# Kernel tuning notes

Hardware: AMD Instinct MI355X
Metric: run time of the kernel (lower is better)

## Reference

```python
import jax, jax.numpy as jnp
import numpy as np

N = 50000
NEG_SLOPE = 0.2  # PyG GATConv default negative_slope


def _gat_layer(x, src, dst, edge_attr, W, We, a_src, a_dst, a_edge, bias):
    """Single-head PyG GATConv (heads=1, concat=True, add_self_loops=True,
    fill_value='mean' for self-loop edge_attr, dropout inactive / eval mode)."""
    n = x.shape[0]
    # add self loops; self-loop edge_attr = per-feature mean of edge_attr
    loop = jnp.arange(n)
    src2 = jnp.concatenate([src, loop])
    dst2 = jnp.concatenate([dst, loop])
    ea_loop = jnp.broadcast_to(edge_attr.mean(axis=0, keepdims=True), (n, edge_attr.shape[1]))
    ea = jnp.concatenate([edge_attr, ea_loop], axis=0)          # [E', edge_dim]

    h = x @ W                                                    # [N, C_out]
    a_s = h @ a_src                                              # [N]
    a_d = h @ a_dst                                              # [N]
    a_e = (ea @ We) @ a_edge                                     # [E']

    alpha = jax.nn.leaky_relu(a_s[src2] + a_d[dst2] + a_e, NEG_SLOPE)  # [E']
    # segment softmax over incoming edges of each dst node
    amax = jax.ops.segment_max(alpha, dst2, num_segments=n)     # [N]
    ex = jnp.exp(alpha - amax[dst2])                             # [E']
    denom = jax.ops.segment_sum(ex, dst2, num_segments=n)       # [N]
    w = ex / denom[dst2]                                         # [E']

    msg = h[src2] * w[:, None]                                   # [E', C_out]
    out = jax.ops.segment_sum(msg, dst2, num_segments=n) + bias  # [N, C_out]
    return out


def setup_inputs() -> dict:
    key = jax.random.key(0)
    ks = jax.random.split(key, 16)
    E, C_in, C_h, C_out, Ed = 800000, 128, 256, 128, 8
    s = 0.05
    inp = {
        "x": jax.random.normal(ks[0], (N, C_in), dtype=jnp.float32),
        "edge_index": jax.random.randint(ks[1], (2, E), 0, N, dtype=jnp.int32),
        "edge_attr": jax.random.normal(ks[2], (E, Ed), dtype=jnp.float32),
        # layer 1 params
        "W1": jax.random.normal(ks[3], (C_in, C_h), dtype=jnp.float32) * s,
        "We1": jax.random.normal(ks[4], (Ed, C_h), dtype=jnp.float32) * s,
        "as1": jax.random.normal(ks[5], (C_h,), dtype=jnp.float32) * s,
        "ad1": jax.random.normal(ks[6], (C_h,), dtype=jnp.float32) * s,
        "ae1": jax.random.normal(ks[7], (C_h,), dtype=jnp.float32) * s,
        "b1": jnp.zeros((C_h,), dtype=jnp.float32),
        # layer 2 params
        "W2": jax.random.normal(ks[8], (C_h, C_out), dtype=jnp.float32) * s,
        "We2": jax.random.normal(ks[9], (Ed, C_out), dtype=jnp.float32) * s,
        "as2": jax.random.normal(ks[10], (C_out,), dtype=jnp.float32) * s,
        "ad2": jax.random.normal(ks[11], (C_out,), dtype=jnp.float32) * s,
        "ae2": jax.random.normal(ks[12], (C_out,), dtype=jnp.float32) * s,
        "b2": jnp.zeros((C_out,), dtype=jnp.float32),
    }
    return inp


def reference(x, edge_index, edge_attr, W1, We1, as1, ad1, ae1, b1,
              W2, We2, as2, ad2, ae2, b2):
    src, dst = edge_index[0], edge_index[1]
    h = _gat_layer(x, src, dst, edge_attr, W1, We1, as1, ad1, ae1, b1)
    h = jax.nn.relu(h)  # relu between layers, not after last
    out = _gat_layer(h, src, dst, edge_attr, W2, We2, as2, ad2, ae2, b2)
    return out
```

## Files before the change

### kernel.cpp

```cpp
#include <hip/hip_runtime.h>
#include <hip/hip_bf16.h>


#define NEG_SLOPE 0.2f
#define EHB 2048

typedef unsigned short u16;
typedef short short8 __attribute__((ext_vector_type(8)));
typedef float v4f __attribute__((ext_vector_type(4)));
typedef u16 u16x4 __attribute__((ext_vector_type(4)));
typedef u16 u16x8 __attribute__((ext_vector_type(8)));

__device__ __forceinline__ u16 f2bf(float f) {
    unsigned u = __float_as_uint(f);
    return (u16)((u + 0x7fffu + ((u >> 16) & 1u)) >> 16);
}
__device__ __forceinline__ float bf2f(u16 h) {
    return __uint_as_float(((unsigned)h) << 16);
}
__device__ __forceinline__ float bf_lo(int v) { return __uint_as_float(((unsigned)v) << 16); }
__device__ __forceinline__ float bf_hi(int v) { return __uint_as_float(((unsigned)v) & 0xffff0000u); }
__device__ __forceinline__ float lrelu(float x) {
    return x >= 0.f ? x : NEG_SLOPE * x;
}
__device__ __forceinline__ int ld_acq(int* p) {
    return __hip_atomic_load(p, __ATOMIC_ACQUIRE, __HIP_MEMORY_SCOPE_AGENT);
}
__device__ __forceinline__ void st_rel(int* p, int v) {
    __hip_atomic_store(p, v, __ATOMIC_RELEASE, __HIP_MEMORY_SCOPE_AGENT);
}

__global__ __launch_bounds__(256) void pre_fat_kernel(
        const float* __restrict__ ea, const int* __restrict__ dst,
        const float* __restrict__ We1, const float* __restrict__ ae1v,
        const float* __restrict__ We2, const float* __restrict__ ae2v,
        float* __restrict__ mean_acc, int* __restrict__ deg,
        int* __restrict__ rank,
        float2* __restrict__ aEe, int E,
        const float* __restrict__ W1, u16* __restrict__ w1thi, u16* __restrict__ w1tlo,
        const float* __restrict__ W2, u16* __restrict__ w2thi, u16* __restrict__ w2tlo,
        float* __restrict__ we_vec1g, float* __restrict__ we_vec2g) {
    int tid = threadIdx.x;
    if (blockIdx.x >= EHB) {
        int t = (blockIdx.x - EHB) * 256 + tid;
        if (t < 128 * 256) {
            int k = t >> 8, m = t & 255;
            float v = W1[t];
            u16 h = f2bf(v);
            w1thi[(size_t)m * 128 + k] = h;
            w1tlo[(size_t)m * 128 + k] = f2bf(v - bf2f(h));
        } else {
            t -= 128 * 256;
            int k = t >> 7, m = t & 127;
            float v = W2[t];
            u16 h = f2bf(v);
            w2thi[(size_t)m * 256 + k] = h;
            w2tlo[(size_t)m * 256 + k] = f2bf(v - bf2f(h));
        }
        return;
    }
    __shared__ float red[8];
    __shared__ float wv[16];
    if (tid < 16) { wv[tid] = 0.f; if (tid < 8) red[tid] = 0.f; }
    __syncthreads();
    {
        float a1 = ae1v[tid];
        int lane = tid & 63;
#pragma unroll
        for (int j = 0; j < 8; ++j) {
            float v = We1[j * 256 + tid] * a1;
#pragma unroll
            for (int o = 32; o; o >>= 1) v += __shfl_down(v, o);
            if (lane == 0) atomicAdd(&wv[j], v);
        }
        if (tid < 128) {
            float a2 = ae2v[tid];
#pragma unroll
            for (int j = 0; j < 8; ++j) {
                float v = We2[j * 128 + tid] * a2;
#pragma unroll
                for (int o = 32; o; o >>= 1) v += __shfl_down(v, o);
                if (lane == 0) atomicAdd(&wv[8 + j], v);
            }
        }
    }
    __syncthreads();
    if (blockIdx.x == 0 && tid < 16) {
        if (tid < 8) we_vec1g[tid] = wv[tid];
        else         we_vec2g[tid - 8] = wv[tid];
    }
    float s[8] = {0.f};
    int stride = EHB * 256;
    for (int e = blockIdx.x * 256 + tid; e < E; e += stride) {
        int d = dst[e];
        rank[e] = atomicAdd(&deg[d], 1);
        const float4 v0 = *(const float4*)&ea[(size_t)e * 8];
        const float4 v1 = *(const float4*)&ea[(size_t)e * 8 + 4];
        s[0] += v0.x; s[1] += v0.y; s[2] += v0.z; s[3] += v0.w;
        s[4] += v1.x; s[5] += v1.y; s[6] += v1.z; s[7] += v1.w;
        float s1 = v0.x * wv[0] + v0.y * wv[1] + v0.z * wv[2] + v0.w * wv[3]
                 + v1.x * wv[4] + v1.y * wv[5] + v1.z * wv[6] + v1.w * wv[7];
        float s2 = v0.x * wv[8] + v0.y * wv[9] + v0.z * wv[10] + v0.w * wv[11]
                 + v1.x * wv[12] + v1.y * wv[13] + v1.z * wv[14] + v1.w * wv[15];
        aEe[e] = make_float2(s1, s2);
    }
#pragma unroll
    for (int j = 0; j < 8; ++j) atomicAdd(&red[j], s[j]);
    __syncthreads();
    if (tid < 8) atomicAdd(&mean_acc[tid], red[tid]);
}

__global__ __launch_bounds__(256) void scan_fused_kernel(
        const int* __restrict__ deg, int* __restrict__ row_start,
        int* __restrict__ partials, int* __restrict__ pprefix,
        int* __restrict__ gcount, int* __restrict__ gflag, int N, int n,
        const float* __restrict__ mean_acc, float Einv,
        const float* __restrict__ we_vec1, const float* __restrict__ we_vec2,
        float* __restrict__ ae_loop) {
    __shared__ int s[256];
    __shared__ int amLast, bprefix;
    int t = threadIdx.x, bid = blockIdx.x;
    int i = bid * 256 + t;
    int v = (i < N) ? deg[i] : 0;
    s[t] = v; __syncthreads();
    for (int off = 1; off < 256; off <<= 1) {
        int u = (t >= off) ? s[t - off] : 0;
        __syncthreads();
        s[t] += u;
        __syncthreads();
    }
    int incl = s[t];
    int total = s[255];
    if (t == 0) {
        partials[bid] = total;
        __threadfence();
        int c = __hip_atomic_fetch_add(gcount, 1, __ATOMIC_ACQ_REL, __HIP_MEMORY_SCOPE_AGENT);
        amLast = (c == (int)gridDim.x - 1);
    }
    __syncthreads();
    if (amLast) {
        int G = gridDim.x;
        int pv = (t < G) ? ld_acq(&partials[t]) : 0;
        __syncthreads();
        s[t] = pv; __syncthreads();
        for (int off = 1; off < 256; off <<= 1) {
            int u = (t >= off) ? s[t - off] : 0;
            __syncthreads();
            s[t] += u;
            __syncthreads();
        }
        if (t < G) pprefix[t] = s[t] - pv;
        if (t == 0) {
            float s1 = 0.f, s2 = 0.f;
#pragma unroll
            for (int j = 0; j < 8; ++j) {
                float m = mean_acc[j] * Einv;
                s1 += m * we_vec1[j];
                s2 += m * we_vec2[j];
            }
            ae_loop[0] = s1; ae_loop[1] = s2;
        }
        __threadfence();
        __syncthreads();
        if (t == 0) st_rel(gflag, 1);
    }
    if (t == 0) {
        while (ld_acq(gflag) == 0) __builtin_amdgcn_s_sleep(2);
        bprefix = ld_acq(&pprefix[bid]);
    }
    __syncthreads();
    int ex = bprefix + incl - v;
    if (i < n) row_start[i] = ex;
}

#define BK 32
#define LDA 40
__global__ __launch_bounds__(256) void gemm1_fill_fat_kernel(
        const float* __restrict__ A32,
        const u16* __restrict__ Bh_g, const u16* __restrict__ Bl_g,
        u16* __restrict__ Cb, int Nrows, int K, int M,
        const float* __restrict__ av, const float* __restrict__ bv,
        float* __restrict__ as_out, float* __restrict__ ad_out, int Gg, int gx,
        const int* __restrict__ src, const int* __restrict__ dst,
        const float2* __restrict__ aEe, const int* __restrict__ row_start,
        const int* __restrict__ rank,
        float4* __restrict__ epack, int E) {
    __shared__ u16 Ah[128 * LDA], Bh[128 * LDA], Bl[128 * LDA];
    int tid = threadIdx.x;
    if ((int)blockIdx.x >= Gg) {
        int e = ((int)blockIdx.x - Gg) * 256 + tid;
        if (e < E) {
            int d = dst[e];
            int idx = row_start[d] + rank[e];
            float2 a = aEe[e];
            epack[idx] = make_float4(__int_as_float(src[e]), a.x, a.y, 0.f);
        }
        return;
    }
    int lane = tid & 63;
    int wv = tid >> 6;
    int wm = wv >> 1, wn = wv & 1;
    int l15 = lane & 15, quad = lane >> 4;
    int rb = ((int)blockIdx.x / gx) * 128;
    int cb = ((int)blockIdx.x % gx) * 128;

    v4f acc[4][4];
#pragma unroll
    for (int mi = 0; mi < 4; ++mi)
#pragma unroll
        for (int ni = 0; ni < 4; ++ni) acc[mi][ni] = (v4f){0.f, 0.f, 0.f, 0.f};

    int sr = tid >> 1;
    int sc = (tid & 1) * 16;

    for (int kc = 0; kc < K; kc += BK) {
        int gr = rb + sr;
        u16x8 a0 = {0,0,0,0,0,0,0,0}, a1 = {0,0,0,0,0,0,0,0};
        if (gr < Nrows) {
            const float* pa = A32 + (size_t)gr * K + kc + sc;
            float4 f0 = *(const float4*)pa;
            float4 f1 = *(const float4*)(pa + 4);
            float4 f2 = *(const float4*)(pa + 8);
            float4 f3 = *(const float4*)(pa + 12);
            a0 = (u16x8){f2bf(f0.x), f2bf(f0.y), f2bf(f0.z), f2bf(f0.w),
                         f2bf(f1.x), f2bf(f1.y), f2bf(f1.z), f2bf(f1.w)};
            a1 = (u16x8){f2bf(f2.x), f2bf(f2.y), f2bf(f2.z), f2bf(f2.w),
                         f2bf(f3.x), f2bf(f3.y), f2bf(f3.z), f2bf(f3.w)};
        }
        size_t bb = (size_t)(cb + sr) * K + kc + sc;
        u16x8 b0 = *(const u16x8*)(Bh_g + bb);
        u16x8 b1 = *(const u16x8*)(Bh_g + bb + 8);
        u16x8 b2 = *(const u16x8*)(Bl_g + bb);
        u16x8 b3 = *(const u16x8*)(Bl_g + bb + 8);
        *(u16x8*)&Ah[sr * LDA + sc] = a0;
        *(u16x8*)&Ah[sr * LDA + sc + 8] = a1;
        *(u16x8*)&Bh[sr * LDA + sc] = b0;
        *(u16x8*)&Bh[sr * LDA + sc + 8] = b1;
        *(u16x8*)&Bl[sr * LDA + sc] = b2;
        *(u16x8*)&Bl[sr * LDA + sc + 8] = b3;
        __syncthreads();
        short8 ah[4], bh[4], bl[4];
#pragma unroll
        for (int mi = 0; mi < 4; ++mi)
            ah[mi] = *(const short8*)&Ah[(wm * 64 + mi * 16 + l15) * LDA + quad * 8];
#pragma unroll
        for (int ni = 0; ni < 4; ++ni) {
            int r = (wn * 64 + ni * 16 + l15) * LDA + quad * 8;
            bh[ni] = *(const short8*)&Bh[r];
            bl[ni] = *(const short8*)&Bl[r];
        }
#pragma unroll
        for (int mi = 0; mi < 4; ++mi)
#pragma unroll
            for (int ni = 0; ni < 4; ++ni) {
                acc[mi][ni] = __builtin_amdgcn_mfma_f32_16x16x32_bf16(ah[mi], bh[ni], acc[mi][ni], 0, 0, 0);
                acc[mi][ni] = __builtin_amdgcn_mfma_f32_16x16x32_bf16(ah[mi], bl[ni], acc[mi][ni], 0, 0, 0);
            }
        __syncthreads();
    }
#pragma unroll
    for (int mi = 0; mi < 4; ++mi)
#pragma unroll
        for (int ni = 0; ni < 4; ++ni)
#pragma unroll
            for (int reg = 0; reg < 4; ++reg) {
                int row = rb + wm * 64 + mi * 16 + quad * 4 + reg;
                if (row < Nrows)
                    Cb[(size_t)row * M + cb + wn * 64 + ni * 16 + l15] = f2bf(acc[mi][ni][reg]);
            }
    float sd[4][4] = {}, dd[4][4] = {};
#pragma unroll
    for (int ni = 0; ni < 4; ++ni) {
        int col = cb + wn * 64 + ni * 16 + l15;
        float a = av[col], b = bv[col];
#pragma unroll
        for (int mi = 0; mi < 4; ++mi)
#pragma unroll
            for (int reg = 0; reg < 4; ++reg) {
                sd[mi][reg] += acc[mi][ni][reg] * a;
                dd[mi][reg] += acc[mi][ni][reg] * b;
            }
    }
#pragma unroll
    for (int off = 1; off < 16; off <<= 1)
#pragma unroll
        for (int mi = 0; mi < 4; ++mi)
#pragma unroll
            for (int reg = 0; reg < 4; ++reg) {
                sd[mi][reg] += __shfl_xor(sd[mi][reg], off);
                dd[mi][reg] += __shfl_xor(dd[mi][reg], off);
            }
    if (l15 == 0)
#pragma unroll
        for (int mi = 0; mi < 4; ++mi) {
            int row0 = rb + wm * 64 + mi * 16 + quad * 4;
#pragma unroll
            for (int reg = 0; reg < 4; ++reg)
                if (row0 + reg < Nrows) {
                    atomicAdd(as_out + row0 + reg, sd[mi][reg]);
                    atomicAdd(ad_out + row0 + reg, dd[mi][reg]);
                }
        }
}

__global__ __launch_bounds__(256) void gemm_mfma_kernel(
        const u16* __restrict__ A_g,
        const u16* __restrict__ Bh_g, const u16* __restrict__ Bl_g,
        u16* __restrict__ Cb, int Nrows, int K, int M,
        const float* __restrict__ av, const float* __restrict__ bv,
        float* __restrict__ as_out, float* __restrict__ ad_out) {
    __shared__ u16 Ah[128 * LDA], Bh[128 * LDA], Bl[128 * LDA];
    int tid = threadIdx.x;
    int lane = tid & 63;
    int wv = tid >> 6;
    int wm = wv >> 1, wn = wv & 1;
    int l15 = lane & 15, quad = lane >> 4;
    int rb = blockIdx.y * 128;
    int cb = blockIdx.x * 128;

    v4f acc[4][4];
#pragma unroll
    for (int mi = 0; mi < 4; ++mi)
#pragma unroll
        for (int ni = 0; ni < 4; ++ni) acc[mi][ni] = (v4f){0.f, 0.f, 0.f, 0.f};

    int sr = tid >> 1;
    int sc = (tid & 1) * 16;

    for (int kc = 0; kc < K; kc += BK) {
        int gr = rb + sr;
        u16x8 a0 = {0,0,0,0,0,0,0,0}, a1 = {0,0,0,0,0,0,0,0};
        if (gr < Nrows) {
            size_t ba = (size_t)gr * K + kc + sc;
            a0 = *(const u16x8*)(A_g + ba);
            a1 = *(const u16x8*)(A_g + ba + 8);
        }
        size_t bb = (size_t)(cb + sr) * K + kc + sc;
        u16x8 b0 = *(const u16x8*)(Bh_g + bb);
        u16x8 b1 = *(const u16x8*)(Bh_g + bb + 8);
        u16x8 b2 = *(const u16x8*)(Bl_g + bb);
        u16x8 b3 = *(const u16x8*)(Bl_g + bb + 8);
        *(u16x8*)&Ah[sr * LDA + sc] = a0;
        *(u16x8*)&Ah[sr * LDA + sc + 8] = a1;
        *(u16x8*)&Bh[sr * LDA + sc] = b0;
        *(u16x8*)&Bh[sr * LDA + sc + 8] = b1;
        *(u16x8*)&Bl[sr * LDA + sc] = b2;
        *(u16x8*)&Bl[sr * LDA + sc + 8] = b3;
        __syncthreads();
        short8 ah[4], bh[4], bl[4];
#pragma unroll
        for (int mi = 0; mi < 4; ++mi)
            ah[mi] = *(const short8*)&Ah[(wm * 64 + mi * 16 + l15) * LDA + quad * 8];
#pragma unroll
        for (int ni = 0; ni < 4; ++ni) {
            int r = (wn * 64 + ni * 16 + l15) * LDA + quad * 8;
            bh[ni] = *(const short8*)&Bh[r];
            bl[ni] = *(const short8*)&Bl[r];
        }
#pragma unroll
        for (int mi = 0; mi < 4; ++mi)
#pragma unroll
            for (int ni = 0; ni < 4; ++ni) {
                acc[mi][ni] = __builtin_amdgcn_mfma_f32_16x16x32_bf16(ah[mi], bh[ni], acc[mi][ni], 0, 0, 0);
                acc[mi][ni] = __builtin_amdgcn_mfma_f32_16x16x32_bf16(ah[mi], bl[ni], acc[mi][ni], 0, 0, 0);
            }
        __syncthreads();
    }
#pragma unroll
    for (int mi = 0; mi < 4; ++mi)
#pragma unroll
        for (int ni = 0; ni < 4; ++ni)
#pragma unroll
            for (int reg = 0; reg < 4; ++reg) {
                int row = rb + wm * 64 + mi * 16 + quad * 4 + reg;
                if (row < Nrows)
                    Cb[(size_t)row * M + cb + wn * 64 + ni * 16 + l15] = f2bf(acc[mi][ni][reg]);
            }
    float sd[4][4] = {}, dd[4][4] = {};
#pragma unroll
    for (int ni = 0; ni < 4; ++ni) {
        int col = cb + wn * 64 + ni * 16 + l15;
        float a = av[col], b = bv[col];
#pragma unroll
        for (int mi = 0; mi < 4; ++mi)
#pragma unroll
            for (int reg = 0; reg < 4; ++reg) {
                sd[mi][reg] += acc[mi][ni][reg] * a;
                dd[mi][reg] += acc[mi][ni][reg] * b;
            }
    }
#pragma unroll
    for (int off = 1; off < 16; off <<= 1)
#pragma unroll
        for (int mi = 0; mi < 4; ++mi)
#pragma unroll
            for (int reg = 0; reg < 4; ++reg) {
                sd[mi][reg] += __shfl_xor(sd[mi][reg], off);
                dd[mi][reg] += __shfl_xor(dd[mi][reg], off);
            }
    if (l15 == 0)
#pragma unroll
        for (int mi = 0; mi < 4; ++mi) {
            int row0 = rb + wm * 64 + mi * 16 + quad * 4;
#pragma unroll
            for (int reg = 0; reg < 4; ++reg)
                if (row0 + reg < Nrows) {
                    atomicAdd(as_out + row0 + reg, sd[mi][reg]);
                    atomicAdd(ad_out + row0 + reg, dd[mi][reg]);
                }
        }
}

__global__ __launch_bounds__(256) void agg1_kernel(const int* __restrict__ row_start,
                                                   const float4* __restrict__ epack,
                                                   const float* __restrict__ asv,
                                                   const float* __restrict__ adv,
                                                   const float* __restrict__ ae_loop,
                                                   const u16* __restrict__ Hb,
                                                   u16* __restrict__ ohi,
                                                   const float* __restrict__ bias, int N) {
    __shared__ float2 xch[4][64];
    int lane = threadIdx.x & 63;
    int wvi = threadIdx.x >> 6;
    int node = blockIdx.x * 4 + wvi;
    if (node >= N) return;
    int st = row_start[node], en = row_start[node + 1];
    float ad = adv[node];
    float aloop = lrelu(asv[node] + ad + ae_loop[0]);
    float m = aloop, sum = 1.f;
    float acc0, acc1, acc2, acc3;
    {
        int2 hv = *(const int2*)(Hb + (size_t)node * 256 + lane * 4);
        acc0 = bf_lo(hv.x); acc1 = bf_hi(hv.x);
        acc2 = bf_lo(hv.y); acc3 = bf_hi(hv.y);
    }
    for (int base = st; base < en; base += 64) {
        int i = base + lane;
        float al = -3.0e38f; int sreg = 0;
        if (i < en) {
            float4 ep = epack[i];
            sreg = __float_as_int(ep.x);
            al = lrelu(asv[sreg] + ad + ep.y);
        }
        float cm = al;
#pragma unroll
        for (int o = 1; o < 64; o <<= 1) cm = fmaxf(cm, __shfl_xor(cm, o));
        if (cm > m) {
            float sc = __expf(m - cm);
            acc0 *= sc; acc1 *= sc; acc2 *= sc; acc3 *= sc;
            sum *= sc; m = cm;
        }
        float w = (i < en) ? __expf(al - m) : 0.f;
        float wsum = w;
#pragma unroll
        for (int o = 1; o < 64; o <<= 1) wsum += __shfl_xor(wsum, o);
        sum += wsum;
        xch[wvi][lane] = make_float2(w, __int_as_float(sreg));
        int cnt = min(64, en - base);
        int j = 0;
        for (; j + 8 <= cnt; j += 8) {
            float2 e[8]; int2 h[8];
#pragma unroll
            for (int q = 0; q < 8; ++q) e[q] = xch[wvi][j + q];
#pragma unroll
            for (int q = 0; q < 8; ++q)
                h[q] = *(const int2*)(Hb + (size_t)__float_as_int(e[q].y) * 256 + lane * 4);
#pragma unroll
            for (int q = 0; q < 8; ++q) {
                acc0 += e[q].x * bf_lo(h[q].x); acc1 += e[q].x * bf_hi(h[q].x);
                acc2 += e[q].x * bf_lo(h[q].y); acc3 += e[q].x * bf_hi(h[q].y);
            }
        }
        for (; j + 4 <= cnt; j += 4) {
            float2 e0 = xch[wvi][j], e1 = xch[wvi][j + 1];
            float2 e2 = xch[wvi][j + 2], e3 = xch[wvi][j + 3];
            int2 h0 = *(const int2*)(Hb + (size_t)__float_as_int(e0.y) * 256 + lane * 4);
            int2 h1 = *(const int2*)(Hb + (size_t)__float_as_int(e1.y) * 256 + lane * 4);
            int2 h2 = *(const int2*)(Hb + (size_t)__float_as_int(e2.y) * 256 + lane * 4);
            int2 h3 = *(const int2*)(Hb + (size_t)__float_as_int(e3.y) * 256 + lane * 4);
            acc0 += e0.x * bf_lo(h0.x) + e1.x * bf_lo(h1.x) + e2.x * bf_lo(h2.x) + e3.x * bf_lo(h3.x);
            acc1 += e0.x * bf_hi(h0.x) + e1.x * bf_hi(h1.x) + e2.x * bf_hi(h2.x) + e3.x * bf_hi(h3.x);
            acc2 += e0.x * bf_lo(h0.y) + e1.x * bf_lo(h1.y) + e2.x * bf_lo(h2.y) + e3.x * bf_lo(h3.y);
            acc3 += e0.x * bf_hi(h0.y) + e1.x * bf_hi(h1.y) + e2.x * bf_hi(h2.y) + e3.x * bf_hi(h3.y);
        }
        for (; j < cnt; ++j) {
            float2 e0 = xch[wvi][j];
            int2 h0 = *(const int2*)(Hb + (size_t)__float_as_int(e0.y) * 256 + lane * 4);
            acc0 += e0.x * bf_lo(h0.x); acc1 += e0.x * bf_hi(h0.x);
            acc2 += e0.x * bf_lo(h0.y); acc3 += e0.x * bf_hi(h0.y);
        }
    }
    float inv = 1.f / sum;
    const float4 bvv = *(const float4*)(bias + lane * 4);
    float t0 = acc0 * inv + bvv.x, t1 = acc1 * inv + bvv.y;
    float t2 = acc2 * inv + bvv.z, t3 = acc3 * inv + bvv.w;
    t0 = t0 > 0.f ? t0 : 0.f; t1 = t1 > 0.f ? t1 : 0.f;
    t2 = t2 > 0.f ? t2 : 0.f; t3 = t3 > 0.f ? t3 : 0.f;
    u16x4 h;
    h.x = f2bf(t0); h.y = f2bf(t1); h.z = f2bf(t2); h.w = f2bf(t3);
    *(u16x4*)(ohi + (size_t)node * 256 + lane * 4) = h;
}

__global__ __launch_bounds__(256) void agg2_kernel(const int* __restrict__ row_start,
                                                   const float4* __restrict__ epack,
                                                   const float* __restrict__ asv,
                                                   const float* __restrict__ adv,
                                                   const float* __restrict__ ae_loop,
                                                   const u16* __restrict__ Hb,
                                                   float* __restrict__ out,
                                                   const float* __restrict__ bias, int N) {
    __shared__ float2 xch[4][64];
    int lane = threadIdx.x & 63;
    int wvi = threadIdx.x >> 6;
    int node = blockIdx.x * 4 + wvi;
    if (node >= N) return;
    int st = row_start[node], en = row_start[node + 1];
    float ad = adv[node];
    float aloop = lrelu(asv[node] + ad + ae_loop[1]);
    float m = aloop, sum = 1.f;
    float acc0, acc1;
    {
        int hv = *(const int*)(Hb + (size_t)node * 128 + lane * 2);
        acc0 = bf_lo(hv); acc1 = bf_hi(hv);
    }
    for (int base = st; base < en; base += 64) {
        int i = base + lane;
        float al = -3.0e38f; int sreg = 0;
        if (i < en) {
            float4 ep = epack[i];
            sreg = __float_as_int(ep.x);
            al = lrelu(asv[sreg] + ad + ep.z);
        }
        float cm = al;
#pragma unroll
        for (int o = 1; o < 64; o <<= 1) cm = fmaxf(cm, __shfl_xor(cm, o));
        if (cm > m) {
            float sc = __expf(m - cm);
            acc0 *= sc; acc1 *= sc;
            sum *= sc; m = cm;
        }
        float w = (i < en) ? __expf(al - m) : 0.f;
        float wsum = w;
#pragma unroll
        for (int o = 1; o < 64; o <<= 1) wsum += __shfl_xor(wsum, o);
        sum += wsum;
        xch[wvi][lane] = make_float2(w, __int_as_float(sreg));
        int cnt = min(64, en - base);
        int j = 0;
        for (; j + 8 <= cnt; j += 8) {
            float2 e[8]; int h[8];
#pragma unroll
            for (int q = 0; q < 8; ++q) e[q] = xch[wvi][j + q];
#pragma unroll
            for (int q = 0; q < 8; ++q)
                h[q] = *(const int*)(Hb + (size_t)__float_as_int(e[q].y) * 128 + lane * 2);
#pragma unroll
            for (int q = 0; q < 8; ++q) {
                acc0 += e[q].x * bf_lo(h[q]); acc1 += e[q].x * bf_hi(h[q]);
            }
        }
        for (; j + 4 <= cnt; j += 4) {
            float2 e0 = xch[wvi][j], e1 = xch[wvi][j + 1];
            float2 e2 = xch[wvi][j + 2], e3 = xch[wvi][j + 3];
            int h0 = *(const int*)(Hb + (size_t)__float_as_int(e0.y) * 128 + lane * 2);
            int h1 = *(const int*)(Hb + (size_t)__float_as_int(e1.y) * 128 + lane * 2);
            int h2 = *(const int*)(Hb + (size_t)__float_as_int(e2.y) * 128 + lane * 2);
            int h3 = *(const int*)(Hb + (size_t)__float_as_int(e3.y) * 128 + lane * 2);
            acc0 += e0.x * bf_lo(h0) + e1.x * bf_lo(h1) + e2.x * bf_lo(h2) + e3.x * bf_lo(h3);
            acc1 += e0.x * bf_hi(h0) + e1.x * bf_hi(h1) + e2.x * bf_hi(h2) + e3.x * bf_hi(h3);
        }
        for (; j < cnt; ++j) {
            float2 e0 = xch[wvi][j];
            int h0 = *(const int*)(Hb + (size_t)__float_as_int(e0.y) * 128 + lane * 2);
            acc0 += e0.x * bf_lo(h0); acc1 += e0.x * bf_hi(h0);
        }
    }
    float inv = 1.f / sum;
    size_t o = (size_t)node * 128 + lane * 2;
    out[o]     = acc0 * inv + bias[lane * 2];
    out[o + 1] = acc1 * inv + bias[lane * 2 + 1];
}

extern "C" void kernel_launch(void* const* d_in, const int* in_sizes, int n_in,
                              void* d_out, int out_size, void* d_ws, size_t ws_size,
                              hipStream_t stream) {
    const int Cin = 128, Ch = 256, Co = 128;
    const int N = in_sizes[0] / Cin;
    const int E = in_sizes[1] / 2;

    const float* x   = (const float*)d_in[0];
    const int*   src = (const int*)d_in[1];
    const int*   dst = src + E;
    const float* ea  = (const float*)d_in[2];
    const float* W1  = (const float*)d_in[3];
    const float* We1 = (const float*)d_in[4];
    const float* as1 = (const float*)d_in[5];
    const float* ad1 = (const float*)d_in[6];
    const float* ae1 = (const float*)d_in[7];
    const float* b1  = (const float*)d_in[8];
    const float* W2  = (const float*)d_in[9];
    const float* We2 = (const float*)d_in[10];
    const float* as2 = (const float*)d_in[11];
    const float* ad2 = (const float*)d_in[12];
    const float* ae2 = (const float*)d_in[13];
    const float* b2  = (const float*)d_in[14];
    float* out = (float*)d_out;

    float* ws = (float*)d_ws;
    size_t off = 0;
    u16* h1b = (u16*)(ws + off); off += (size_t)N * Ch / 2;
    u16* g1b = (u16*)(ws + off); off += (size_t)N * Ch / 2;
    float4* epack = (float4*)(ws + off); off += (size_t)E * 4;
    float2* aEe   = (float2*)(ws + off); off += (size_t)E * 2;
    int* rank     = (int*)(ws + off); off += (size_t)E;
    int* row_start = (int*)(ws + off); off += (size_t)N + 1;
    int* partials  = (int*)(ws + off); off += 256;
    int* pprefix   = (int*)(ws + off); off += 256;
    u16* w1thi = (u16*)(ws + off); off += (size_t)Cin * Ch / 2;
    u16* w1tlo = (u16*)(ws + off); off += (size_t)Cin * Ch / 2;
    u16* w2thi = (u16*)(ws + off); off += (size_t)Ch * Co / 2;
    u16* w2tlo = (u16*)(ws + off); off += (size_t)Ch * Co / 2;
    int*   deg  = (int*)(ws + off); off += (size_t)N + 1;
    float* asv1 = ws + off; off += (size_t)N;
    float* adv1 = ws + off; off += (size_t)N;
    float* asv2 = ws + off; off += (size_t)N;
    float* adv2 = ws + off; off += (size_t)N;
    float* misc = ws + off; off += 32;
    float* mean_acc = misc;
    float* we_vec1  = misc + 8;
    float* we_vec2  = misc + 16;
    float* ae_loop  = misc + 24;
    int* gcount = (int*)(ws + off); off += 1;
    int* gflag  = (int*)(ws + off); off += 1;

    const int n1 = N + 1;
    const int nscan = (n1 + 255) / 256;

    hipMemsetAsync(deg, 0, ((size_t)5 * N + 35) * sizeof(float), stream);

    pre_fat_kernel<<<EHB + 256, 256, 0, stream>>>(
        ea, dst, We1, ae1, We2, ae2, mean_acc, deg, rank, aEe, E,
        W1, w1thi, w1tlo, W2, w2thi, w2tlo, we_vec1, we_vec2);

    scan_fused_kernel<<<nscan, 256, 0, stream>>>(
        deg, row_start, partials, pprefix, gcount, gflag, N, n1,
        mean_acc, 1.0f / (float)E, we_vec1, we_vec2, ae_loop);

    {
        int gx = Ch / 128;
        int Gg = gx * ((N + 127) / 128);
        int Fb = (E + 255) / 256;
        gemm1_fill_fat_kernel<<<Gg + Fb, 256, 0, stream>>>(
            x, w1thi, w1tlo, h1b, N, Cin, Ch, as1, ad1, asv1, adv1, Gg, gx,
            src, dst, aEe, row_start, rank, epack, E);
    }
    agg1_kernel<<<(N + 3) / 4, 256, 0, stream>>>(row_start, epack, asv1, adv1, ae_loop,
                                                 h1b, g1b, b1, N);

    u16* h2b = h1b;
    {
        dim3 grid(Co / 128, (N + 127) / 128);
        gemm_mfma_kernel<<<grid, 256, 0, stream>>>(g1b, w2thi, w2tlo, h2b, N, Ch, Co,
                                                   as2, ad2, asv2, adv2);
    }
    agg2_kernel<<<(N + 3) / 4, 256, 0, stream>>>(row_start, epack, asv2, adv2, ae_loop,
                                                 h2b, out, b2, N);
}
```

Before: 386.8 us.

## Co-schedule edge preprocessing with layer-1 GEMM and split fill into own kernel

The weight transpose/split and edge-weight vector computation move into a small prep kernel. The per-edge pass (degree counting, rank, edge-attention precompute, edge_attr mean) is now fused into the same launch as the layer-1 GEMM, one edge per thread with wave-level shuffle reductions, while the CSR fill becomes a standalone kernel after the scan. The aim is to overlap the atomic-heavy edge pass with the compute-bound GEMM, at the cost of one extra kernel launch and a larger fused grid.

```diff
diff --git a/kernel.cpp b/kernel.cpp
--- a/kernel.cpp
+++ b/kernel.cpp
@@ -3,7 +3,6 @@
 
 
 #define NEG_SLOPE 0.2f
-#define EHB 2048
 
 typedef unsigned short u16;
 typedef short short8 __attribute__((ext_vector_type(8)));
@@ -30,19 +29,15 @@
     __hip_atomic_store(p, v, __ATOMIC_RELEASE, __HIP_MEMORY_SCOPE_AGENT);
 }
 
-__global__ __launch_bounds__(256) void pre_fat_kernel(
-        const float* __restrict__ ea, const int* __restrict__ dst,
+__global__ __launch_bounds__(256) void prep_kernel(
+        const float* __restrict__ W1, u16* __restrict__ w1thi, u16* __restrict__ w1tlo,
+        const float* __restrict__ W2, u16* __restrict__ w2thi, u16* __restrict__ w2tlo,
         const float* __restrict__ We1, const float* __restrict__ ae1v,
         const float* __restrict__ We2, const float* __restrict__ ae2v,
-        float* __restrict__ mean_acc, int* __restrict__ deg,
-        int* __restrict__ rank,
-        float2* __restrict__ aEe, int E,
-        const float* __restrict__ W1, u16* __restrict__ w1thi, u16* __restrict__ w1tlo,
-        const float* __restrict__ W2, u16* __restrict__ w2thi, u16* __restrict__ w2tlo,
         float* __restrict__ we_vec1g, float* __restrict__ we_vec2g) {
     int tid = threadIdx.x;
-    if (blockIdx.x >= EHB) {
-        int t = (blockIdx.x - EHB) * 256 + tid;
+    if (blockIdx.x < 256) {
+        int t = blockIdx.x * 256 + tid;
         if (t < 128 * 256) {
             int k = t >> 8, m = t & 255;
             float v = W1[t];
@@ -59,9 +54,8 @@
         }
         return;
     }
-    __shared__ float red[8];
     __shared__ float wv[16];
-    if (tid < 16) { wv[tid] = 0.f; if (tid < 8) red[tid] = 0.f; }
+    if (tid < 16) wv[tid] = 0.f;
     __syncthreads();
     {
         float a1 = ae1v[tid];
@@ -85,29 +79,162 @@
         }
     }
     __syncthreads();
-    if (blockIdx.x == 0 && tid < 16) {
-        if (tid < 8) we_vec1g[tid] = wv[tid];
-        else         we_vec2g[tid - 8] = wv[tid];
-    }
-    float s[8] = {0.f};
-    int stride = EHB * 256;
-    for (int e = blockIdx.x * 256 + tid; e < E; e += stride) {
-        int d = dst[e];
-        rank[e] = atomicAdd(&deg[d], 1);
-        const float4 v0 = *(const float4*)&ea[(size_t)e * 8];
-        const float4 v1 = *(const float4*)&ea[(size_t)e * 8 + 4];
-        s[0] += v0.x; s[1] += v0.y; s[2] += v0.z; s[3] += v0.w;
-        s[4] += v1.x; s[5] += v1.y; s[6] += v1.z; s[7] += v1.w;
-        float s1 = v0.x * wv[0] + v0.y * wv[1] + v0.z * wv[2] + v0.w * wv[3]
-                 + v1.x * wv[4] + v1.y * wv[5] + v1.z * wv[6] + v1.w * wv[7];
-        float s2 = v0.x * wv[8] + v0.y * wv[9] + v0.z * wv[10] + v0.w * wv[11]
-                 + v1.x * wv[12] + v1.y * wv[13] + v1.z * wv[14] + v1.w * wv[15];
-        aEe[e] = make_float2(s1, s2);
-    }
-#pragma unroll
-    for (int j = 0; j < 8; ++j) atomicAdd(&red[j], s[j]);
-    __syncthreads();
-    if (tid < 8) atomicAdd(&mean_acc[tid], red[tid]);
+    if (tid < 8)  we_vec1g[tid] = wv[tid];
+    else if (tid < 16) we_vec2g[tid - 8] = wv[tid];
+}
+
+#define BK 32
+#define LDA 40
+__global__ __launch_bounds__(256) void fat1_kernel(
+        const float* __restrict__ ea, const int* __restrict__ dst,
+        float* __restrict__ mean_acc, int* __restrict__ deg,
+        int* __restrict__ rank, float2* __restrict__ aEe, int E,
+        const float* __restrict__ we_vec1g, const float* __restrict__ we_vec2g,
+        int Fb,
+        const float* __restrict__ A32,
+        const u16* __restrict__ Bh_g, const u16* __restrict__ Bl_g,
+        u16* __restrict__ Cb, int Nrows, int K, int M,
+        const float* __restrict__ av, const float* __restrict__ bv,
+        float* __restrict__ as_out, float* __restrict__ ad_out, int gx) {
+    __shared__ u16 Ah[128 * LDA], Bh[128 * LDA], Bl[128 * LDA];
+    int tid = threadIdx.x;
+    if ((int)blockIdx.x < Fb) {
+        __shared__ float red[8];
+        __shared__ float wv[16];
+        if (tid < 16) { wv[tid] = (tid < 8) ? we_vec1g[tid] : we_vec2g[tid - 8];
+                        if (tid < 8) red[tid] = 0.f; }
+        __syncthreads();
+        int e = (int)blockIdx.x * 256 + tid;
+        float s[8] = {0.f};
+        if (e < E) {
+            const float4 v0 = *(const float4*)&ea[(size_t)e * 8];
+            const float4 v1 = *(const float4*)&ea[(size_t)e * 8 + 4];
+            int d = dst[e];
+            s[0] = v0.x; s[1] = v0.y; s[2] = v0.z; s[3] = v0.w;
+            s[4] = v1.x; s[5] = v1.y; s[6] = v1.z; s[7] = v1.w;
+            float s1 = v0.x * wv[0] + v0.y * wv[1] + v0.z * wv[2] + v0.w * wv[3]
+                     + v1.x * wv[4] + v1.y * wv[5] + v1.z * wv[6] + v1.w * wv[7];
+            float s2 = v0.x * wv[8] + v0.y * wv[9] + v0.z * wv[10] + v0.w * wv[11]
+                     + v1.x * wv[12] + v1.y * wv[13] + v1.z * wv[14] + v1.w * wv[15];
+            aEe[e] = make_float2(s1, s2);
+            rank[e] = atomicAdd(&deg[d], 1);
+        }
+        int lane = tid & 63;
+#pragma unroll
+        for (int j = 0; j < 8; ++j) {
+#pragma unroll
+            for (int o = 32; o; o >>= 1) s[j] += __shfl_down(s[j], o);
+            if (lane == 0) atomicAdd(&red[j], s[j]);
+        }
+        __syncthreads();
+        if (tid < 8) atomicAdd(&mean_acc[tid], red[tid]);
+        return;
+    }
+    int gb = (int)blockIdx.x - Fb;
+    int lane = tid & 63;
+    int wvx = tid >> 6;
+    int wm = wvx >> 1, wn = wvx & 1;
+    int l15 = lane & 15, quad = lane >> 4;
+    int rb = (gb / gx) * 128;
+    int cb = (gb % gx) * 128;
+
+    v4f acc[4][4];
+#pragma unroll
+    for (int mi = 0; mi < 4; ++mi)
+#pragma unroll
+        for (int ni = 0; ni < 4; ++ni) acc[mi][ni] = (v4f){0.f, 0.f, 0.f, 0.f};
+
+    int sr = tid >> 1;
+    int sc = (tid & 1) * 16;
+
+    for (int kc = 0; kc < K; kc += BK) {
+        int gr = rb + sr;
+        u16x8 a0 = {0,0,0,0,0,0,0,0}, a1 = {0,0,0,0,0,0,0,0};
+        if (gr < Nrows) {
+            const float* pa = A32 + (size_t)gr * K + kc + sc;
+            float4 f0 = *(const float4*)pa;
+            float4 f1 = *(const float4*)(pa + 4);
+            float4 f2 = *(const float4*)(pa + 8);
+            float4 f3 = *(const float4*)(pa + 12);
+            a0 = (u16x8){f2bf(f0.x), f2bf(f0.y), f2bf(f0.z), f2bf(f0.w),
+                         f2bf(f1.x), f2bf(f1.y), f2bf(f1.z), f2bf(f1.w)};
+            a1 = (u16x8){f2bf(f2.x), f2bf(f2.y), f2bf(f2.z), f2bf(f2.w),
+                         f2bf(f3.x), f2bf(f3.y), f2bf(f3.z), f2bf(f3.w)};
+        }
+        size_t bb = (size_t)(cb + sr) * K + kc + sc;
+        u16x8 b0 = *(const u16x8*)(Bh_g + bb);
+        u16x8 b1 = *(const u16x8*)(Bh_g + bb + 8);
+        u16x8 b2 = *(const u16x8*)(Bl_g + bb);
+        u16x8 b3 = *(const u16x8*)(Bl_g + bb + 8);
+        *(u16x8*)&Ah[sr * LDA + sc] = a0;
+        *(u16x8*)&Ah[sr * LDA + sc + 8] = a1;
+        *(u16x8*)&Bh[sr * LDA + sc] = b0;
+        *(u16x8*)&Bh[sr * LDA + sc + 8] = b1;
+        *(u16x8*)&Bl[sr * LDA + sc] = b2;
+        *(u16x8*)&Bl[sr * LDA + sc + 8] = b3;
+        __syncthreads();
+        short8 ah[4], bh[4], bl[4];
+#pragma unroll
+        for (int mi = 0; mi < 4; ++mi)
+            ah[mi] = *(const short8*)&Ah[(wm * 64 + mi * 16 + l15) * LDA + quad * 8];
+#pragma unroll
+        for (int ni = 0; ni < 4; ++ni) {
+            int r = (wn * 64 + ni * 16 + l15) * LDA + quad * 8;
+            bh[ni] = *(const short8*)&Bh[r];
+            bl[ni] = *(const short8*)&Bl[r];
+        }
+#pragma unroll
+        for (int mi = 0; mi < 4; ++mi)
+#pragma unroll
+            for (int ni = 0; ni < 4; ++ni) {
+                acc[mi][ni] = __builtin_amdgcn_mfma_f32_16x16x32_bf16(ah[mi], bh[ni], acc[mi][ni], 0, 0, 0);
+                acc[mi][ni] = __builtin_amdgcn_mfma_f32_16x16x32_bf16(ah[mi], bl[ni], acc[mi][ni], 0, 0, 0);
+            }
+        __syncthreads();
+    }
+#pragma unroll
+    for (int mi = 0; mi < 4; ++mi)
+#pragma unroll
+        for (int ni = 0; ni < 4; ++ni)
+#pragma unroll
+            for (int reg = 0; reg < 4; ++reg) {
+                int row = rb + wm * 64 + mi * 16 + quad * 4 + reg;
+                if (row < Nrows)
+                    Cb[(size_t)row * M + cb + wn * 64 + ni * 16 + l15] = f2bf(acc[mi][ni][reg]);
+            }
+    float sd[4][4] = {}, dd[4][4] = {};
+#pragma unroll
+    for (int ni = 0; ni < 4; ++ni) {
+        int col = cb + wn * 64 + ni * 16 + l15;
+        float a = av[col], b = bv[col];
+#pragma unroll
+        for (int mi = 0; mi < 4; ++mi)
+#pragma unroll
+            for (int reg = 0; reg < 4; ++reg) {
+                sd[mi][reg] += acc[mi][ni][reg] * a;
+                dd[mi][reg] += acc[mi][ni][reg] * b;
+            }
+    }
+#pragma unroll
+    for (int off = 1; off < 16; off <<= 1)
+#pragma unroll
+        for (int mi = 0; mi < 4; ++mi)
+#pragma unroll
+            for (int reg = 0; reg < 4; ++reg) {
+                sd[mi][reg] += __shfl_xor(sd[mi][reg], off);
+                dd[mi][reg] += __shfl_xor(dd[mi][reg], off);
+            }
+    if (l15 == 0)
+#pragma unroll
+        for (int mi = 0; mi < 4; ++mi) {
+            int row0 = rb + wm * 64 + mi * 16 + quad * 4;
+#pragma unroll
+            for (int reg = 0; reg < 4; ++reg)
+                if (row0 + reg < Nrows) {
+                    atomicAdd(as_out + row0 + reg, sd[mi][reg]);
+                    atomicAdd(ad_out + row0 + reg, dd[mi][reg]);
+                }
+        }
 }
 
 __global__ __launch_bounds__(256) void scan_fused_kernel(
@@ -173,134 +300,17 @@
     if (i < n) row_start[i] = ex;
 }
 
-#define BK 32
-#define LDA 40
-__global__ __launch_bounds__(256) void gemm1_fill_fat_kernel(
-        const float* __restrict__ A32,
-        const u16* __restrict__ Bh_g, const u16* __restrict__ Bl_g,
-        u16* __restrict__ Cb, int Nrows, int K, int M,
-        const float* __restrict__ av, const float* __restrict__ bv,
-        float* __restrict__ as_out, float* __restrict__ ad_out, int Gg, int gx,
+__global__ __launch_bounds__(256) void fill_kernel(
         const int* __restrict__ src, const int* __restrict__ dst,
         const float2* __restrict__ aEe, const int* __restrict__ row_start,
         const int* __restrict__ rank,
         float4* __restrict__ epack, int E) {
-    __shared__ u16 Ah[128 * LDA], Bh[128 * LDA], Bl[128 * LDA];
-    int tid = threadIdx.x;
-    if ((int)blockIdx.x >= Gg) {
-        int e = ((int)blockIdx.x - Gg) * 256 + tid;
-        if (e < E) {
-            int d = dst[e];
-            int idx = row_start[d] + rank[e];
-            float2 a = aEe[e];
-            epack[idx] = make_float4(__int_as_float(src[e]), a.x, a.y, 0.f);
-        }
-        return;
-    }
-    int lane = tid & 63;
-    int wv = tid >> 6;
-    int wm = wv >> 1, wn = wv & 1;
-    int l15 = lane & 15, quad = lane >> 4;
-    int rb = ((int)blockIdx.x / gx) * 128;
-    int cb = ((int)blockIdx.x % gx) * 128;
-
-    v4f acc[4][4];
-#pragma unroll
-    for (int mi = 0; mi < 4; ++mi)
-#pragma unroll
-        for (int ni = 0; ni < 4; ++ni) acc[mi][ni] = (v4f){0.f, 0.f, 0.f, 0.f};
-
-    int sr = tid >> 1;
-    int sc = (tid & 1) * 16;
-
-    for (int kc = 0; kc < K; kc += BK) {
-        int gr = rb + sr;
-        u16x8 a0 = {0,0,0,0,0,0,0,0}, a1 = {0,0,0,0,0,0,0,0};
-        if (gr < Nrows) {
-            const float* pa = A32 + (size_t)gr * K + kc + sc;
-            float4 f0 = *(const float4*)pa;
-            float4 f1 = *(const float4*)(pa + 4);
-            float4 f2 = *(const float4*)(pa + 8);
-            float4 f3 = *(const float4*)(pa + 12);
-            a0 = (u16x8){f2bf(f0.x), f2bf(f0.y), f2bf(f0.z), f2bf(f0.w),
-                         f2bf(f1.x), f2bf(f1.y), f2bf(f1.z), f2bf(f1.w)};
-            a1 = (u16x8){f2bf(f2.x), f2bf(f2.y), f2bf(f2.z), f2bf(f2.w),
-                         f2bf(f3.x), f2bf(f3.y), f2bf(f3.z), f2bf(f3.w)};
-        }
-        size_t bb = (size_t)(cb + sr) * K + kc + sc;
-        u16x8 b0 = *(const u16x8*)(Bh_g + bb);
-        u16x8 b1 = *(const u16x8*)(Bh_g + bb + 8);
-        u16x8 b2 = *(const u16x8*)(Bl_g + bb);
-        u16x8 b3 = *(const u16x8*)(Bl_g + bb + 8);
-        *(u16x8*)&Ah[sr * LDA + sc] = a0;
-        *(u16x8*)&Ah[sr * LDA + sc + 8] = a1;
-        *(u16x8*)&Bh[sr * LDA + sc] = b0;
-        *(u16x8*)&Bh[sr * LDA + sc + 8] = b1;
-        *(u16x8*)&Bl[sr * LDA + sc] = b2;
-        *(u16x8*)&Bl[sr * LDA + sc + 8] = b3;
-        __syncthreads();
-        short8 ah[4], bh[4], bl[4];
-#pragma unroll
-        for (int mi = 0; mi < 4; ++mi)
-            ah[mi] = *(const short8*)&Ah[(wm * 64 + mi * 16 + l15) * LDA + quad * 8];
-#pragma unroll
-        for (int ni = 0; ni < 4; ++ni) {
-            int r = (wn * 64 + ni * 16 + l15) * LDA + quad * 8;
-            bh[ni] = *(const short8*)&Bh[r];
-            bl[ni] = *(const short8*)&Bl[r];
-        }
-#pragma unroll
-        for (int mi = 0; mi < 4; ++mi)
-#pragma unroll
-            for (int ni = 0; ni < 4; ++ni) {
-                acc[mi][ni] = __builtin_amdgcn_mfma_f32_16x16x32_bf16(ah[mi], bh[ni], acc[mi][ni], 0, 0, 0);
-                acc[mi][ni] = __builtin_amdgcn_mfma_f32_16x16x32_bf16(ah[mi], bl[ni], acc[mi][ni], 0, 0, 0);
-            }
-        __syncthreads();
-    }
-#pragma unroll
-    for (int mi = 0; mi < 4; ++mi)
-#pragma unroll
-        for (int ni = 0; ni < 4; ++ni)
-#pragma unroll
-            for (int reg = 0; reg < 4; ++reg) {
-                int row = rb + wm * 64 + mi * 16 + quad * 4 + reg;
-                if (row < Nrows)
-                    Cb[(size_t)row * M + cb + wn * 64 + ni * 16 + l15] = f2bf(acc[mi][ni][reg]);
-            }
-    float sd[4][4] = {}, dd[4][4] = {};
-#pragma unroll
-    for (int ni = 0; ni < 4; ++ni) {
-        int col = cb + wn * 64 + ni * 16 + l15;
-        float a = av[col], b = bv[col];
-#pragma unroll
-        for (int mi = 0; mi < 4; ++mi)
-#pragma unroll
-            for (int reg = 0; reg < 4; ++reg) {
-                sd[mi][reg] += acc[mi][ni][reg] * a;
-                dd[mi][reg] += acc[mi][ni][reg] * b;
-            }
-    }
-#pragma unroll
-    for (int off = 1; off < 16; off <<= 1)
-#pragma unroll
-        for (int mi = 0; mi < 4; ++mi)
-#pragma unroll
-            for (int reg = 0; reg < 4; ++reg) {
-                sd[mi][reg] += __shfl_xor(sd[mi][reg], off);
-                dd[mi][reg] += __shfl_xor(dd[mi][reg], off);
-            }
-    if (l15 == 0)
-#pragma unroll
-        for (int mi = 0; mi < 4; ++mi) {
-            int row0 = rb + wm * 64 + mi * 16 + quad * 4;
-#pragma unroll
-            for (int reg = 0; reg < 4; ++reg)
-                if (row0 + reg < Nrows) {
-                    atomicAdd(as_out + row0 + reg, sd[mi][reg]);
-                    atomicAdd(ad_out + row0 + reg, dd[mi][reg]);
-                }
-        }
+    int e = blockIdx.x * 256 + threadIdx.x;
+    if (e >= E) return;
+    int d = dst[e];
+    int idx = row_start[d] + rank[e];
+    float2 a = aEe[e];
+    epack[idx] = make_float4(__int_as_float(src[e]), a.x, a.y, 0.f);
 }
 
 __global__ __launch_bounds__(256) void gemm_mfma_kernel(
@@ -638,22 +648,26 @@
 
     hipMemsetAsync(deg, 0, ((size_t)5 * N + 35) * sizeof(float), stream);
 
-    pre_fat_kernel<<<EHB + 256, 256, 0, stream>>>(
-        ea, dst, We1, ae1, We2, ae2, mean_acc, deg, rank, aEe, E,
-        W1, w1thi, w1tlo, W2, w2thi, w2tlo, we_vec1, we_vec2);
+    prep_kernel<<<257, 256, 0, stream>>>(
+        W1, w1thi, w1tlo, W2, w2thi, w2tlo,
+        We1, ae1, We2, ae2, we_vec1, we_vec2);
+
+    {
+        int Fb = (E + 255) / 256;
+        int gx = Ch / 128;
+        int Gg = gx * ((N + 127) / 128);
+        fat1_kernel<<<Fb + Gg, 256, 0, stream>>>(
+            ea, dst, mean_acc, deg, rank, aEe, E, we_vec1, we_vec2, Fb,
+            x, w1thi, w1tlo, h1b, N, Cin, Ch, as1, ad1, asv1, adv1, gx);
+    }
 
     scan_fused_kernel<<<nscan, 256, 0, stream>>>(
         deg, row_start, partials, pprefix, gcount, gflag, N, n1,
         mean_acc, 1.0f / (float)E, we_vec1, we_vec2, ae_loop);
 
-    {
-        int gx = Ch / 128;
-        int Gg = gx * ((N + 127) / 128);
-        int Fb = (E + 255) / 256;
-        gemm1_fill_fat_kernel<<<Gg + Fb, 256, 0, stream>>>(
-            x, w1thi, w1tlo, h1b, N, Cin, Ch, as1, ad1, asv1, adv1, Gg, gx,
-            src, dst, aEe, row_start, rank, epack, E);
-    }
+    fill_kernel<<<(E + 255) / 256, 256, 0, stream>>>(src, dst, aEe, row_start,
+                                                     rank, epack, E);
+
     agg1_kernel<<<(N + 3) / 4, 256, 0, stream>>>(row_start, epack, asv1, adv1, ae_loop,
                                                  h1b, g1b, b1, N);
 
```

After: 432.4 us. +11.8%, slower.
